# Kernel optimization log

Hardware: AMD Instinct MI355X
Metric: run time of the kernel (lower is better)

The kernel has to match this reference:

```python
import jax, jax.numpy as jnp
import numpy as np

HIDDEN = 768  # hidden_dim of the embedding matrix
VOCAB = 30522


def setup_inputs() -> dict:
    key = jax.random.key(0)
    k1, k2, k3, k4, k5, k6 = jax.random.split(key, 6)
    core = jax.random.normal(k1, (40, 256, 256), dtype=jnp.float32)
    f0 = jax.random.normal(k2, (40, 40), dtype=jnp.float32)
    f1 = jax.random.normal(k3, (768, 256), dtype=jnp.float32)
    f2 = jax.random.normal(k4, (768, 256), dtype=jnp.float32)
    ids = jax.random.randint(k5, (8192,), 0, VOCAB, dtype=jnp.int32)
    x = jax.random.normal(k6, (8192, 768), dtype=jnp.float32)  # unused by forward, kept for signature parity
    return {"x": x, "ids": ids, "core": core, "f0": f0, "f1": f1, "f2": f2}


def reference(x, ids, core, f0, f1, f2):
    # tucker_to_tensor: core x_0 f0 x_1 f1 x_2 f2 -> (40, 768, 768)
    res = jnp.einsum('abc,ia,jb,kc->ijk', core, f0, f1, f2)
    # flatten to padded embedding table (30720, 768) and gather requested rows
    table = res.reshape(-1, HIDDEN)
    return table[ids, :]
```

## Files before the change

kernel.cpp:

```cpp
#include <hip/hip_runtime.h>


#define A_DIM 40
#define BC 65536
#define C_DIM 256
#define HID 768

typedef __attribute__((ext_vector_type(8))) short short8;
typedef __attribute__((ext_vector_type(4))) float floatx4;

#define AS1 __attribute__((address_space(1)))
#define AS3 __attribute__((address_space(3)))

__device__ __forceinline__ void gl2lds16(const unsigned short* g, unsigned short* l) {
    __builtin_amdgcn_global_load_lds((const AS1 unsigned int*)g, (AS3 unsigned int*)l,
                                     16, 0, 0);
}

__device__ __forceinline__ unsigned short f2bf(float f) {
    unsigned int u = __builtin_bit_cast(unsigned int, f);
    u += 0x7FFFu + ((u >> 16) & 1u);
    return (unsigned short)(u >> 16);
}

__global__ __launch_bounds__(256) void k01_cvt_mode0(const float* __restrict__ core,
                                                     const float* __restrict__ f0,
                                                     const float* __restrict__ f1,
                                                     const float* __restrict__ f2,
                                                     unsigned short* __restrict__ A1,
                                                     unsigned short* __restrict__ f1b,
                                                     unsigned short* __restrict__ f2b) {
    const int bid = blockIdx.x;
    if (bid < 1024) {
        __shared__ float f0s[A_DIM * A_DIM];
        const int i0 = (bid >> 8) * 10;
        for (int e = threadIdx.x; e < A_DIM * A_DIM; e += 256) f0s[e] = f0[e];
        __syncthreads();
        const int bc = (bid & 255) * 256 + threadIdx.x;
        float acc[10];
#pragma unroll
        for (int ii = 0; ii < 10; ++ii) acc[ii] = 0.f;
        for (int a = 0; a < A_DIM; ++a) {
            const float cv = core[a * BC + bc];
#pragma unroll
            for (int ii = 0; ii < 10; ++ii) acc[ii] += f0s[(i0 + ii) * A_DIM + a] * cv;
        }
#pragma unroll
        for (int ii = 0; ii < 10; ++ii) A1[(i0 + ii) * BC + bc] = f2bf(acc[ii]);
    } else {
        const int idx = (bid - 1024) * 256 + threadIdx.x;
        const float* src;
        unsigned short* dst;
        int off;
        if (idx < 49152) { src = f1; dst = f1b; off = idx; }
        else             { src = f2; dst = f2b; off = idx - 49152; }
        const float4 v = *(const float4*)&src[off * 4];
        const unsigned int lo = (unsigned int)f2bf(v.x) | ((unsigned int)f2bf(v.y) << 16);
        const unsigned int hi = (unsigned int)f2bf(v.z) | ((unsigned int)f2bf(v.w) << 16);
        *(uint2*)&dst[off * 4] = make_uint2(lo, hi);
    }
}

__global__ __launch_bounds__(256) void k1_transpose(const unsigned short* __restrict__ A1,
                                                    unsigned short* __restrict__ A1t) {
    const int i  = blockIdx.z;
    const int b0 = blockIdx.x * 64;
    const int c0 = blockIdx.y * 64;
    const unsigned short* __restrict__ src = A1 + i * BC;
    unsigned short* __restrict__ dst = A1t + i * BC;
    __shared__ unsigned short tile[64 * 66];
    const int t = threadIdx.x;
#pragma unroll
    for (int h = 0; h < 2; ++h) {
        const int s = t + h * 256;
        const int r = s >> 3, cs = (s & 7) * 8;
        short8 v = *(const short8*)&src[(b0 + r) * 256 + c0 + cs];
#pragma unroll
        for (int u = 0; u < 8; ++u) tile[r * 66 + cs + u] = ((unsigned short*)&v)[u];
    }
    __syncthreads();
#pragma unroll
    for (int h = 0; h < 2; ++h) {
        const int s = t + h * 256;
        const int c = s >> 3, bs = (s & 7) * 8;
        short8 o;
#pragma unroll
        for (int u = 0; u < 8; ++u) ((unsigned short*)&o)[u] = tile[(bs + u) * 66 + c];
        *(short8*)&dst[(c0 + c) * 256 + b0 + bs] = o;
    }
}

__global__ __launch_bounds__(256) void k2_gemm(const unsigned short* __restrict__ f1b,
                                               const unsigned short* __restrict__ A1t,
                                               unsigned short* __restrict__ A2) {
    const int i  = blockIdx.z;
    const int j0 = blockIdx.x * 64;
    const int c0 = blockIdx.y * 64;
    const unsigned short* __restrict__ Bsrc = A1t + i * BC;

    __shared__ unsigned short As[64 * 32];
    __shared__ unsigned short Bs[64 * 32];

    const int tid = threadIdx.x;
    const int lane = tid & 63, wave = tid >> 6;
    const int wm = (wave >> 1) * 32, wn = (wave & 1) * 32;
    const int l16 = lane & 15, q = lane >> 4;

    const int r0 = tid >> 2, o0 = (tid & 3) * 8;
    unsigned short* AsW = &As[wave * 512];
    unsigned short* BsW = &Bs[wave * 512];

    floatx4 acc[2][2];
#pragma unroll
    for (int p = 0; p < 2; ++p)
#pragma unroll
        for (int r = 0; r < 2; ++r) acc[p][r] = (floatx4)0.f;

    for (int kk = 0; kk < C_DIM; kk += 32) {
        gl2lds16(&f1b[(j0 + r0) * 256 + kk + o0], AsW);
        gl2lds16(&Bsrc[(c0 + r0) * 256 + kk + o0], BsW);
        __syncthreads();
        short8 af[2], bf[2];
#pragma unroll
        for (int p = 0; p < 2; ++p) af[p] = *(const short8*)&As[(wm + p * 16 + l16) * 32 + q * 8];
#pragma unroll
        for (int r = 0; r < 2; ++r) bf[r] = *(const short8*)&Bs[(wn + r * 16 + l16) * 32 + q * 8];
#pragma unroll
        for (int p = 0; p < 2; ++p)
#pragma unroll
            for (int r = 0; r < 2; ++r)
                acc[p][r] = __builtin_amdgcn_mfma_f32_16x16x32_bf16(af[p], bf[r], acc[p][r], 0, 0, 0);
        __syncthreads();
    }
    unsigned short* __restrict__ Cout = A2 + (size_t)i * HID * C_DIM;
#pragma unroll
    for (int p = 0; p < 2; ++p)
#pragma unroll
        for (int r = 0; r < 2; ++r)
#pragma unroll
            for (int rr = 0; rr < 4; ++rr) {
                const int row = j0 + wm + p * 16 + q * 4 + rr;
                const int col = c0 + wn + r * 16 + l16;
                Cout[row * 256 + col] = f2bf(acc[p][r][rr]);
            }
}

__global__ __launch_bounds__(256) void k3_gemm(const unsigned short* __restrict__ A2,
                                               const unsigned short* __restrict__ f2b,
                                               const int* __restrict__ ids,
                                               float* __restrict__ out) {
    const int n0 = blockIdx.x * 64;
    const int k0 = blockIdx.y * 64;

    __shared__ int ids_s[64];
    __shared__ unsigned short As[64 * 32];
    __shared__ unsigned short Bs[64 * 32];

    const int tid = threadIdx.x;
    if (tid < 64) ids_s[tid] = ids[n0 + tid];
    __syncthreads();

    const int lane = tid & 63, wave = tid >> 6;
    const int wm = (wave >> 1) * 32, wn = (wave & 1) * 32;
    const int l16 = lane & 15, q = lane >> 4;

    const int r0 = tid >> 2, o0 = (tid & 3) * 8;
    const size_t ga = (size_t)ids_s[r0] * 256;
    unsigned short* AsW = &As[wave * 512];
    unsigned short* BsW = &Bs[wave * 512];

    floatx4 acc[2][2];
#pragma unroll
    for (int p = 0; p < 2; ++p)
#pragma unroll
        for (int r = 0; r < 2; ++r) acc[p][r] = (floatx4)0.f;

    for (int kk = 0; kk < C_DIM; kk += 32) {
        gl2lds16(&A2[ga + kk + o0], AsW);
        gl2lds16(&f2b[(k0 + r0) * 256 + kk + o0], BsW);
        __syncthreads();
        short8 af[2], bf[2];
#pragma unroll
        for (int p = 0; p < 2; ++p) af[p] = *(const short8*)&As[(wm + p * 16 + l16) * 32 + q * 8];
#pragma unroll
        for (int r = 0; r < 2; ++r) bf[r] = *(const short8*)&Bs[(wn + r * 16 + l16) * 32 + q * 8];
#pragma unroll
        for (int p = 0; p < 2; ++p)
#pragma unroll
            for (int r = 0; r < 2; ++r)
                acc[p][r] = __builtin_amdgcn_mfma_f32_16x16x32_bf16(af[p], bf[r], acc[p][r], 0, 0, 0);
        __syncthreads();
    }
#pragma unroll
    for (int p = 0; p < 2; ++p)
#pragma unroll
        for (int r = 0; r < 2; ++r)
#pragma unroll
            for (int rr = 0; rr < 4; ++rr) {
                const int row = n0 + wm + p * 16 + q * 4 + rr;
                const int col = k0 + wn + r * 16 + l16;
                out[(size_t)row * HID + col] = acc[p][r][rr];
            }
}

extern "C" void kernel_launch(void* const* d_in, const int* in_sizes, int n_in,
                              void* d_out, int out_size, void* d_ws, size_t ws_size,
                              hipStream_t stream) {
    const int*   ids  = (const int*)d_in[1];
    const float* core = (const float*)d_in[2];
    const float* f0   = (const float*)d_in[3];
    const float* f1   = (const float*)d_in[4];
    const float* f2   = (const float*)d_in[5];
    float* out = (float*)d_out;

    char* ws = (char*)d_ws;
    unsigned short* A1  = (unsigned short*)ws;
    unsigned short* A1t = (unsigned short*)(ws + 5242880);
    unsigned short* A2  = (unsigned short*)(ws + 10485760);
    unsigned short* f1b = (unsigned short*)(ws + 26214400);
    unsigned short* f2b = (unsigned short*)(ws + 26607616);

    k01_cvt_mode0<<<1408, 256, 0, stream>>>(core, f0, f1, f2, A1, f1b, f2b);
    k1_transpose<<<dim3(4, 4, A_DIM), 256, 0, stream>>>(A1, A1t);
    k2_gemm<<<dim3(12, 4, A_DIM), 256, 0, stream>>>(f1b, A1t, A2);
    k3_gemm<<<dim3(128, 12), 256, 0, stream>>>(A2, f2b, ids, out);
}
```

Before: 118.3 us.

## Fuse mode-0 contraction with transpose through LDS, dropping the separate transpose kernel

The mode-0 contraction kernel now works on 32x32 (b,c) tiles, 5 output slices per block, with 2x2 elements per thread. It transposes the bf16 results through a small LDS tile and writes A1t directly. This removes the k1_transpose launch and its extra write and read of the 5 MB intermediate. In exchange core is re-read 8 times instead of 4, with narrower float2 loads, and there are fewer blocks (512 compute blocks) plus extra barriers per slice.

Measured after the change: 113.5 us (median of 2 runs). 4.1% less time.

```diff
diff --git a/kernel.cpp b/kernel.cpp
--- a/kernel.cpp
+++ b/kernel.cpp
@@ -23,32 +23,68 @@
     return (unsigned short)(u >> 16);
 }
 
-__global__ __launch_bounds__(256) void k01_cvt_mode0(const float* __restrict__ core,
-                                                     const float* __restrict__ f0,
-                                                     const float* __restrict__ f1,
-                                                     const float* __restrict__ f2,
-                                                     unsigned short* __restrict__ A1,
-                                                     unsigned short* __restrict__ f1b,
-                                                     unsigned short* __restrict__ f2b) {
+__global__ __launch_bounds__(256) void k01_fused(const float* __restrict__ core,
+                                                 const float* __restrict__ f0,
+                                                 const float* __restrict__ f1,
+                                                 const float* __restrict__ f2,
+                                                 unsigned short* __restrict__ A1t,
+                                                 unsigned short* __restrict__ f1b,
+                                                 unsigned short* __restrict__ f2b) {
     const int bid = blockIdx.x;
-    if (bid < 1024) {
-        __shared__ float f0s[A_DIM * A_DIM];
-        const int i0 = (bid >> 8) * 10;
-        for (int e = threadIdx.x; e < A_DIM * A_DIM; e += 256) f0s[e] = f0[e];
-        __syncthreads();
-        const int bc = (bid & 255) * 256 + threadIdx.x;
-        float acc[10];
-#pragma unroll
-        for (int ii = 0; ii < 10; ++ii) acc[ii] = 0.f;
+    const int tid = threadIdx.x;
+    if (bid < 512) {
+        __shared__ float f0s[200];
+        __shared__ unsigned short tt[32 * 34];
+        const int i0 = (bid >> 6) * 5;
+        const int tile = bid & 63;
+        const int b0 = (tile >> 3) * 32;
+        const int c0 = (tile & 7) * 32;
+        if (tid < 200) f0s[tid] = f0[i0 * A_DIM + tid];
+        __syncthreads();
+
+        const int pb = (tid >> 4) * 2;
+        const int pc = (tid & 15) * 2;
+        float acc[5][4];
+#pragma unroll
+        for (int ii = 0; ii < 5; ++ii)
+#pragma unroll
+            for (int e = 0; e < 4; ++e) acc[ii][e] = 0.f;
+
+        const float* cp0 = core + (b0 + pb) * 256 + (c0 + pc);
         for (int a = 0; a < A_DIM; ++a) {
-            const float cv = core[a * BC + bc];
-#pragma unroll
-            for (int ii = 0; ii < 10; ++ii) acc[ii] += f0s[(i0 + ii) * A_DIM + a] * cv;
+            const float* cp = cp0 + a * BC;
+            const float2 r0 = *(const float2*)cp;
+            const float2 r1 = *(const float2*)(cp + 256);
+#pragma unroll
+            for (int ii = 0; ii < 5; ++ii) {
+                const float fa = f0s[ii * A_DIM + a];
+                acc[ii][0] += fa * r0.x;
+                acc[ii][1] += fa * r0.y;
+                acc[ii][2] += fa * r1.x;
+                acc[ii][3] += fa * r1.y;
+            }
         }
-#pragma unroll
-        for (int ii = 0; ii < 10; ++ii) A1[(i0 + ii) * BC + bc] = f2bf(acc[ii]);
+        const int rc = tid >> 3;
+        const int rb4 = (tid & 7) * 4;
+#pragma unroll
+        for (int ii = 0; ii < 5; ++ii) {
+            if (ii) __syncthreads();
+            unsigned short e00 = f2bf(acc[ii][0]);
+            unsigned short e10 = f2bf(acc[ii][2]);
+            unsigned short e01 = f2bf(acc[ii][1]);
+            unsigned short e11 = f2bf(acc[ii][3]);
+            *(unsigned int*)&tt[pc * 34 + pb]       = (unsigned int)e00 | ((unsigned int)e10 << 16);
+            *(unsigned int*)&tt[(pc + 1) * 34 + pb] = (unsigned int)e01 | ((unsigned int)e11 << 16);
+            __syncthreads();
+            unsigned short o[4];
+#pragma unroll
+            for (int u = 0; u < 4; ++u) o[u] = tt[rc * 34 + rb4 + u];
+            unsigned int lo = (unsigned int)o[0] | ((unsigned int)o[1] << 16);
+            unsigned int hi = (unsigned int)o[2] | ((unsigned int)o[3] << 16);
+            *(uint2*)&A1t[(size_t)(i0 + ii) * BC + (c0 + rc) * 256 + b0 + rb4] = make_uint2(lo, hi);
+        }
     } else {
-        const int idx = (bid - 1024) * 256 + threadIdx.x;
+        const int idx = (bid - 512) * 256 + tid;
         const float* src;
         unsigned short* dst;
         int off;
@@ -61,35 +97,6 @@
     }
 }
 
-__global__ __launch_bounds__(256) void k1_transpose(const unsigned short* __restrict__ A1,
-                                                    unsigned short* __restrict__ A1t) {
-    const int i  = blockIdx.z;
-    const int b0 = blockIdx.x * 64;
-    const int c0 = blockIdx.y * 64;
-    const unsigned short* __restrict__ src = A1 + i * BC;
-    unsigned short* __restrict__ dst = A1t + i * BC;
-    __shared__ unsigned short tile[64 * 66];
-    const int t = threadIdx.x;
-#pragma unroll
-    for (int h = 0; h < 2; ++h) {
-        const int s = t + h * 256;
-        const int r = s >> 3, cs = (s & 7) * 8;
-        short8 v = *(const short8*)&src[(b0 + r) * 256 + c0 + cs];
-#pragma unroll
-        for (int u = 0; u < 8; ++u) tile[r * 66 + cs + u] = ((unsigned short*)&v)[u];
-    }
-    __syncthreads();
-#pragma unroll
-    for (int h = 0; h < 2; ++h) {
-        const int s = t + h * 256;
-        const int c = s >> 3, bs = (s & 7) * 8;
-        short8 o;
-#pragma unroll
-        for (int u = 0; u < 8; ++u) ((unsigned short*)&o)[u] = tile[(bs + u) * 66 + c];
-        *(short8*)&dst[(c0 + c) * 256 + b0 + bs] = o;
-    }
-}
-
 __global__ __launch_bounds__(256) void k2_gemm(const unsigned short* __restrict__ f1b,
                                                const unsigned short* __restrict__ A1t,
                                                unsigned short* __restrict__ A2) {
@@ -214,14 +221,12 @@
     float* out = (float*)d_out;
 
     char* ws = (char*)d_ws;
-    unsigned short* A1  = (unsigned short*)ws;
-    unsigned short* A1t = (unsigned short*)(ws + 5242880);
-    unsigned short* A2  = (unsigned short*)(ws + 10485760);
-    unsigned short* f1b = (unsigned short*)(ws + 26214400);
-    unsigned short* f2b = (unsigned short*)(ws + 26607616);
-
-    k01_cvt_mode0<<<1408, 256, 0, stream>>>(core, f0, f1, f2, A1, f1b, f2b);
-    k1_transpose<<<dim3(4, 4, A_DIM), 256, 0, stream>>>(A1, A1t);
+    unsigned short* A1t = (unsigned short*)ws;
+    unsigned short* A2  = (unsigned short*)(ws + 5242880);
+    unsigned short* f1b = (unsigned short*)(ws + 20971520);
+    unsigned short* f2b = (unsigned short*)(ws + 21364736);
+
+    k01_fused<<<896, 256, 0, stream>>>(core, f0, f1, f2, A1t, f1b, f2b);
     k2_gemm<<<dim3(12, 4, A_DIM), 256, 0, stream>>>(f1b, A1t, A2);
     k3_gemm<<<dim3(128, 12), 256, 0, stream>>>(A2, f2b, ids, out);
 }
```
